# Kernel tuning notes

Hardware: AMD Instinct MI355X
Metric: run time of the kernel (lower is better)

The kernel has to match this reference:

```python
import jax, jax.numpy as jnp
import numpy as np

B = 16384
F_IN = 768
F_OUT = 512

def setup_inputs() -> dict:
    key = jax.random.key(0)
    k1, k2, k3, k4, k5, k6 = jax.random.split(key, 6)
    # densified sparse multi-hot boards (post to_dense())
    stm = jax.random.uniform(k1, (B, F_IN), dtype=jnp.float32)
    nstm = jax.random.uniform(k2, (B, F_IN), dtype=jnp.float32)
    s1 = 1.0 / np.sqrt(F_IN)
    s2 = 1.0 / np.sqrt(2 * F_OUT)
    W1 = jax.random.normal(k3, (F_OUT, F_IN), dtype=jnp.float32) * s1
    b1 = jax.random.normal(k4, (F_OUT,), dtype=jnp.float32) * s1
    W2 = jax.random.normal(k5, (1, 2 * F_OUT), dtype=jnp.float32) * s2
    b2 = jax.random.normal(k6, (1,), dtype=jnp.float32) * s2
    return {"stm": stm, "nstm": nstm, "W1": W1, "b1": b1, "W2": W2, "b2": b2}

def reference(stm, nstm, W1, b1, W2, b2):
    # shared feature transformer applied to both perspectives
    stm_p = stm @ W1.T + b1    # [B, F_OUT]
    nstm_p = nstm @ W1.T + b1  # [B, F_OUT]
    hidden = jnp.clip(jnp.concatenate((stm_p, nstm_p), axis=1), 0.0, 1.0)  # [B, 2*F_OUT]
    return jax.nn.sigmoid(hidden @ W2.T + b2)  # [B, 1]
```

## Files before the change

kernel.cpp:

```cpp
#include <hip/hip_runtime.h>
#include <hip/hip_bf16.h>

#define BATCH 16384
#define FIN   768
#define FOUT  512

#define BK 64
#define NT (FIN / BK)
#define BM 128
#define BN 256

typedef __attribute__((ext_vector_type(8))) short short8;
typedef __attribute__((ext_vector_type(4))) float floatx4;

__device__ __forceinline__ unsigned int cvt_pk_bf16(float a, float b) {
    unsigned int r;
    asm("v_cvt_pk_bf16_f32 %0, %1, %2" : "=v"(r) : "v"(a), "v"(b));
    return r;
}

__device__ __forceinline__ void load_lds_16(const void* g, void* l) {
    __builtin_amdgcn_global_load_lds(
        (const __attribute__((address_space(1))) unsigned int*)g,
        (__attribute__((address_space(3))) unsigned int*)l,
        16, 0, 0);
}

__global__ __launch_bounds__(256) void cvt_w1(
    const float* __restrict__ W1, unsigned short* __restrict__ W1b)
{
    int base = (blockIdx.x * 256 + threadIdx.x) * 8;
    float4 a = *(const float4*)(W1 + base);
    float4 b = *(const float4*)(W1 + base + 4);
    uint4 o;
    o.x = cvt_pk_bf16(a.x, a.y); o.y = cvt_pk_bf16(a.z, a.w);
    o.z = cvt_pk_bf16(b.x, b.y); o.w = cvt_pk_bf16(b.z, b.w);
    *(uint4*)(W1b + base) = o;
}

__global__ __launch_bounds__(1024, 4) void pn_gemm(
    const float* __restrict__ stm, const float* __restrict__ nstm,
    const unsigned short* __restrict__ W1b, const float* __restrict__ b1,
    const float* __restrict__ W2, float* __restrict__ P)
{
    __shared__ __align__(16) unsigned short As[2][256 * 64];
    __shared__ __align__(16) unsigned short Bs[2][256 * 64];

    const int tid  = threadIdx.x;
    const int lane = tid & 63;
    const int wave = tid >> 6;
    const int wr   = wave >> 2;
    const int wc   = wave & 3;
    const int quad = lane >> 4;
    const int l16  = lane & 15;

    const int bm    = blockIdx.x >> 1;
    const int n_idx = blockIdx.x & 1;
    const int b0    = bm * BM;
    const int n0    = n_idx * BN;

    const int arow = tid >> 2;
    const int ac   = tid & 3;
    const float* aSrc =
        ((arow < BM) ? stm  + (size_t)(b0 + arow) * FIN
                     : nstm + (size_t)(b0 + arow - BM) * FIN);
    const int aOffLo = arow * 64 + ((ac       ^ (arow & 7)) * 8);
    const int aOffHi = arow * 64 + (((ac + 4) ^ (arow & 7)) * 8);

    const int brow = lane >> 3;
    const int bch  = (lane & 7) ^ brow;
    const unsigned short* bSrc =
        W1b + (size_t)(n0 + brow) * FIN + bch * 8;

    floatx4 acc[4][4];
    #pragma unroll
    for (int i = 0; i < 4; ++i)
        #pragma unroll
        for (int j = 0; j < 4; ++j)
            acc[i][j] = (floatx4)0.0f;

    float4 ap0 = *(const float4*)(aSrc + ac * 8);
    float4 ap1 = *(const float4*)(aSrc + ac * 8 + 4);
    float4 ap2 = *(const float4*)(aSrc + (ac + 4) * 8);
    float4 ap3 = *(const float4*)(aSrc + (ac + 4) * 8 + 4);
    #pragma unroll
    for (int i = 0; i < 2; ++i) {
        const int J = wave * 2 + i;
        load_lds_16(bSrc + (size_t)(J * 8) * FIN, &Bs[0][J * 512]);
    }

    for (int t = 0; t < NT; ++t) {
        const int cur = t & 1;
        const int nxt = cur ^ 1;

        {
            uint4 o1, o2;
            o1.x = cvt_pk_bf16(ap0.x, ap0.y); o1.y = cvt_pk_bf16(ap0.z, ap0.w);
            o1.z = cvt_pk_bf16(ap1.x, ap1.y); o1.w = cvt_pk_bf16(ap1.z, ap1.w);
            o2.x = cvt_pk_bf16(ap2.x, ap2.y); o2.y = cvt_pk_bf16(ap2.z, ap2.w);
            o2.z = cvt_pk_bf16(ap3.x, ap3.y); o2.w = cvt_pk_bf16(ap3.z, ap3.w);
            *(uint4*)(&As[cur][aOffLo]) = o1;
            *(uint4*)(&As[cur][aOffHi]) = o2;
        }
        __syncthreads();

        if (t + 1 < NT) {
            const int kn = (t + 1) * BK;
            #pragma unroll
            for (int i = 0; i < 2; ++i) {
                const int J = wave * 2 + i;
                load_lds_16(bSrc + (size_t)(J * 8) * FIN + kn, &Bs[nxt][J * 512]);
            }
            ap0 = *(const float4*)(aSrc + kn + ac * 8);
            ap1 = *(const float4*)(aSrc + kn + ac * 8 + 4);
            ap2 = *(const float4*)(aSrc + kn + (ac + 4) * 8);
            ap3 = *(const float4*)(aSrc + kn + (ac + 4) * 8 + 4);
        }

        #pragma unroll
        for (int kk = 0; kk < 2; ++kk) {
            const int c = kk * 4 + quad;
            short8 af[4], bfr[4];
            #pragma unroll
            for (int mi = 0; mi < 4; ++mi) {
                const int m = wr * 64 + mi * 16 + l16;
                af[mi] = *(const short8*)(&As[cur][m * 64 + ((c ^ (m & 7)) * 8)]);
            }
            #pragma unroll
            for (int ni = 0; ni < 4; ++ni) {
                const int n = wc * 64 + ni * 16 + l16;
                bfr[ni] = *(const short8*)(&Bs[cur][n * 64 + ((c ^ (n & 7)) * 8)]);
            }
            #pragma unroll
            for (int mi = 0; mi < 4; ++mi)
                #pragma unroll
                for (int ni = 0; ni < 4; ++ni)
                    acc[mi][ni] = __builtin_amdgcn_mfma_f32_16x16x32_bf16(
                        af[mi], bfr[ni], acc[mi][ni], 0, 0, 0);
        }
    }

    float b1v[4], w2v[4];
    const float* w2base = (wr < 2) ? W2 : W2 + FOUT;
    #pragma unroll
    for (int ni = 0; ni < 4; ++ni) {
        int col = n0 + wc * 64 + ni * 16 + l16;
        b1v[ni] = b1[col];
        w2v[ni] = w2base[col];
    }

    __syncthreads();
    float* Epi = (float*)As;

    #pragma unroll
    for (int mi = 0; mi < 4; ++mi) {
        #pragma unroll
        for (int r = 0; r < 4; ++r) {
            float s = 0.0f;
            #pragma unroll
            for (int ni = 0; ni < 4; ++ni) {
                float h = acc[mi][ni][r] + b1v[ni];
                h = fminf(fmaxf(h, 0.0f), 1.0f);
                s += h * w2v[ni];
            }
            s += __shfl_xor(s, 1);
            s += __shfl_xor(s, 2);
            s += __shfl_xor(s, 4);
            s += __shfl_xor(s, 8);
            if (l16 == 0) {
                Epi[(wr * 64 + mi * 16 + quad * 4 + r) * 4 + wc] = s;
            }
        }
    }
    __syncthreads();

    if (tid < BM) {
        float x = 0.0f;
        #pragma unroll
        for (int j = 0; j < 4; ++j)
            x += Epi[tid * 4 + j] + Epi[(tid + BM) * 4 + j];
        P[n_idx * BATCH + b0 + tid] = x;
    }
}

__global__ __launch_bounds__(256) void finish(
    const float* __restrict__ P, const float* __restrict__ b2,
    float* __restrict__ out)
{
    int i = blockIdx.x * 256 + threadIdx.x;
    float x = b2[0] + P[i] + P[BATCH + i];
    out[i] = 1.0f / (1.0f + expf(-x));
}

extern "C" void kernel_launch(void* const* d_in, const int* in_sizes, int n_in,
                              void* d_out, int out_size, void* d_ws, size_t ws_size,
                              hipStream_t stream)
{
    (void)in_sizes; (void)n_in; (void)out_size; (void)ws_size;
    const float* stm  = (const float*)d_in[0];
    const float* nstm = (const float*)d_in[1];
    const float* W1   = (const float*)d_in[2];
    const float* b1   = (const float*)d_in[3];
    const float* W2   = (const float*)d_in[4];
    const float* b2   = (const float*)d_in[5];
    float* out = (float*)d_out;
    unsigned short* W1b = (unsigned short*)d_ws;
    float* P = (float*)((char*)d_ws + FOUT * FIN * 2);

    cvt_w1<<<dim3((FOUT * FIN) / (256 * 8)), dim3(256), 0, stream>>>(W1, W1b);
    pn_gemm<<<dim3((BATCH / BM) * 2), dim3(1024), 0, stream>>>(
        stm, nstm, W1b, b1, W2, P);
    finish<<<dim3(BATCH / 256), dim3(256), 0, stream>>>(P, b2, out);
}
```

Measured before the change: 146.2 us.

## Halve block to 512 threads with 8x4 MFMA tiles per wave, remap block ids, set MFMA priority

Drops the GEMM block from 16 to 8 waves. Each wave now computes a 128x64 output tile (8x4 MFMA accumulators) and each thread loads twice as much of A and B per stage. This gives more reuse of the B fragments per LDS read and fewer waves competing per block. Block ids are remapped (blockIdx & 7)*32 + (blockIdx >> 3), likely to place related tiles on the same XCD for cache locality, and s_setprio is raised around the MFMA bursts. The cost is higher register pressure from 128 accumulator floats per thread, which could lower occupancy.

```diff
diff --git a/kernel.cpp b/kernel.cpp
--- a/kernel.cpp
+++ b/kernel.cpp
@@ -38,7 +38,7 @@
     *(uint4*)(W1b + base) = o;
 }
 
-__global__ __launch_bounds__(1024, 4) void pn_gemm(
+__global__ __launch_bounds__(512, 2) void pn_gemm(
     const float* __restrict__ stm, const float* __restrict__ nstm,
     const unsigned short* __restrict__ W1b, const float* __restrict__ b1,
     const float* __restrict__ W2, float* __restrict__ P)
@@ -54,38 +54,43 @@
     const int quad = lane >> 4;
     const int l16  = lane & 15;
 
-    const int bm    = blockIdx.x >> 1;
-    const int n_idx = blockIdx.x & 1;
+    const int sbid  = (blockIdx.x & 7) * 32 + (blockIdx.x >> 3);
+    const int bm    = sbid >> 1;
+    const int n_idx = sbid & 1;
     const int b0    = bm * BM;
     const int n0    = n_idx * BN;
 
-    const int arow = tid >> 2;
-    const int ac   = tid & 3;
+    const int arow = tid >> 1;
+    const int h    = tid & 1;
     const float* aSrc =
         ((arow < BM) ? stm  + (size_t)(b0 + arow) * FIN
-                     : nstm + (size_t)(b0 + arow - BM) * FIN);
-    const int aOffLo = arow * 64 + ((ac       ^ (arow & 7)) * 8);
-    const int aOffHi = arow * 64 + (((ac + 4) ^ (arow & 7)) * 8);
+                     : nstm + (size_t)(b0 + arow - BM) * FIN) + h * 32;
+    int aOff[4];
+    #pragma unroll
+    for (int c = 0; c < 4; ++c)
+        aOff[c] = arow * 64 + (((h * 4 + c) ^ (arow & 7)) * 8);
 
     const int brow = lane >> 3;
     const int bch  = (lane & 7) ^ brow;
     const unsigned short* bSrc =
         W1b + (size_t)(n0 + brow) * FIN + bch * 8;
 
-    floatx4 acc[4][4];
-    #pragma unroll
-    for (int i = 0; i < 4; ++i)
+    floatx4 acc[8][4];
+    #pragma unroll
+    for (int i = 0; i < 8; ++i)
         #pragma unroll
         for (int j = 0; j < 4; ++j)
             acc[i][j] = (floatx4)0.0f;
 
-    float4 ap0 = *(const float4*)(aSrc + ac * 8);
-    float4 ap1 = *(const float4*)(aSrc + ac * 8 + 4);
-    float4 ap2 = *(const float4*)(aSrc + (ac + 4) * 8);
-    float4 ap3 = *(const float4*)(aSrc + (ac + 4) * 8 + 4);
-    #pragma unroll
-    for (int i = 0; i < 2; ++i) {
-        const int J = wave * 2 + i;
+    float4 ap[8];
+    #pragma unroll
+    for (int c = 0; c < 4; ++c) {
+        ap[2 * c]     = *(const float4*)(aSrc + c * 8);
+        ap[2 * c + 1] = *(const float4*)(aSrc + c * 8 + 4);
+    }
+    #pragma unroll
+    for (int i = 0; i < 4; ++i) {
+        const int J = wave * 4 + i;
         load_lds_16(bSrc + (size_t)(J * 8) * FIN, &Bs[0][J * 512]);
     }
 
@@ -93,37 +98,38 @@
         const int cur = t & 1;
         const int nxt = cur ^ 1;
 
-        {
-            uint4 o1, o2;
-            o1.x = cvt_pk_bf16(ap0.x, ap0.y); o1.y = cvt_pk_bf16(ap0.z, ap0.w);
-            o1.z = cvt_pk_bf16(ap1.x, ap1.y); o1.w = cvt_pk_bf16(ap1.z, ap1.w);
-            o2.x = cvt_pk_bf16(ap2.x, ap2.y); o2.y = cvt_pk_bf16(ap2.z, ap2.w);
-            o2.z = cvt_pk_bf16(ap3.x, ap3.y); o2.w = cvt_pk_bf16(ap3.z, ap3.w);
-            *(uint4*)(&As[cur][aOffLo]) = o1;
-            *(uint4*)(&As[cur][aOffHi]) = o2;
+        #pragma unroll
+        for (int c = 0; c < 4; ++c) {
+            uint4 o;
+            o.x = cvt_pk_bf16(ap[2 * c].x, ap[2 * c].y);
+            o.y = cvt_pk_bf16(ap[2 * c].z, ap[2 * c].w);
+            o.z = cvt_pk_bf16(ap[2 * c + 1].x, ap[2 * c + 1].y);
+            o.w = cvt_pk_bf16(ap[2 * c + 1].z, ap[2 * c + 1].w);
+            *(uint4*)(&As[cur][aOff[c]]) = o;
         }
         __syncthreads();
 
         if (t + 1 < NT) {
             const int kn = (t + 1) * BK;
             #pragma unroll
-            for (int i = 0; i < 2; ++i) {
-                const int J = wave * 2 + i;
+            for (int c = 0; c < 4; ++c) {
+                ap[2 * c]     = *(const float4*)(aSrc + kn + c * 8);
+                ap[2 * c + 1] = *(const float4*)(aSrc + kn + c * 8 + 4);
+            }
+            #pragma unroll
+            for (int i = 0; i < 4; ++i) {
+                const int J = wave * 4 + i;
                 load_lds_16(bSrc + (size_t)(J * 8) * FIN + kn, &Bs[nxt][J * 512]);
             }
-            ap0 = *(const float4*)(aSrc + kn + ac * 8);
-            ap1 = *(const float4*)(aSrc + kn + ac * 8 + 4);
-            ap2 = *(const float4*)(aSrc + kn + (ac + 4) * 8);
-            ap3 = *(const float4*)(aSrc + kn + (ac + 4) * 8 + 4);
         }
 
         #pragma unroll
         for (int kk = 0; kk < 2; ++kk) {
             const int c = kk * 4 + quad;
-            short8 af[4], bfr[4];
-            #pragma unroll
-            for (int mi = 0; mi < 4; ++mi) {
-                const int m = wr * 64 + mi * 16 + l16;
+            short8 af[8], bfr[4];
+            #pragma unroll
+            for (int mi = 0; mi < 8; ++mi) {
+                const int m = wr * 128 + mi * 16 + l16;
                 af[mi] = *(const short8*)(&As[cur][m * 64 + ((c ^ (m & 7)) * 8)]);
             }
             #pragma unroll
@@ -131,17 +137,19 @@
                 const int n = wc * 64 + ni * 16 + l16;
                 bfr[ni] = *(const short8*)(&Bs[cur][n * 64 + ((c ^ (n & 7)) * 8)]);
             }
-            #pragma unroll
-            for (int mi = 0; mi < 4; ++mi)
+            __builtin_amdgcn_s_setprio(1);
+            #pragma unroll
+            for (int mi = 0; mi < 8; ++mi)
                 #pragma unroll
                 for (int ni = 0; ni < 4; ++ni)
                     acc[mi][ni] = __builtin_amdgcn_mfma_f32_16x16x32_bf16(
                         af[mi], bfr[ni], acc[mi][ni], 0, 0, 0);
+            __builtin_amdgcn_s_setprio(0);
         }
     }
 
     float b1v[4], w2v[4];
-    const float* w2base = (wr < 2) ? W2 : W2 + FOUT;
+    const float* w2base = (wr == 0) ? W2 : W2 + FOUT;
     #pragma unroll
     for (int ni = 0; ni < 4; ++ni) {
         int col = n0 + wc * 64 + ni * 16 + l16;
@@ -153,22 +161,22 @@
     float* Epi = (float*)As;
 
     #pragma unroll
-    for (int mi = 0; mi < 4; ++mi) {
+    for (int mi = 0; mi < 8; ++mi) {
         #pragma unroll
         for (int r = 0; r < 4; ++r) {
             float s = 0.0f;
             #pragma unroll
             for (int ni = 0; ni < 4; ++ni) {
-                float h = acc[mi][ni][r] + b1v[ni];
-                h = fminf(fmaxf(h, 0.0f), 1.0f);
-                s += h * w2v[ni];
+                float hh = acc[mi][ni][r] + b1v[ni];
+                hh = fminf(fmaxf(hh, 0.0f), 1.0f);
+                s += hh * w2v[ni];
             }
             s += __shfl_xor(s, 1);
             s += __shfl_xor(s, 2);
             s += __shfl_xor(s, 4);
             s += __shfl_xor(s, 8);
             if (l16 == 0) {
-                Epi[(wr * 64 + mi * 16 + quad * 4 + r) * 4 + wc] = s;
+                Epi[(wr * 128 + mi * 16 + quad * 4 + r) * 4 + wc] = s;
             }
         }
     }
@@ -208,7 +216,7 @@
     float* P = (float*)((char*)d_ws + FOUT * FIN * 2);
 
     cvt_w1<<<dim3((FOUT * FIN) / (256 * 8)), dim3(256), 0, stream>>>(W1, W1b);
-    pn_gemm<<<dim3((BATCH / BM) * 2), dim3(1024), 0, stream>>>(
+    pn_gemm<<<dim3((BATCH / BM) * 2), dim3(512), 0, stream>>>(
         stm, nstm, W1b, b1, W2, P);
     finish<<<dim3(BATCH / 256), dim3(256), 0, stream>>>(P, b2, out);
 }
```

New measurement: 163.7 us. 1.12x slower.

## Triple-buffer W1 tiles with prefetch distance two and swizzle block order

Applied to the files above, without the earlier changes.

Moves the W1 tile to three LDS buffers and issues its async global-to-LDS loads two k-steps ahead. The block barrier is replaced by a custom one that waits with vmcnt(2), so the newest B prefetch can stay in flight across the barrier. Block indices are also remapped so that neighbouring tiles spread across XCD groups. The aim is to hide global load latency of the B operand, at the cost of raising LDS use to 160KB and relying on a hand-counted vmcnt being correct.

```diff
diff --git a/kernel.cpp b/kernel.cpp
--- a/kernel.cpp
+++ b/kernel.cpp
@@ -25,6 +25,13 @@
         (__attribute__((address_space(3))) unsigned int*)l,
         16, 0, 0);
 }
+
+#define BAR_VM2() do {                                               \
+    __builtin_amdgcn_sched_barrier(0);                               \
+    asm volatile("s_waitcnt vmcnt(2) lgkmcnt(0)" ::: "memory");      \
+    __builtin_amdgcn_s_barrier();                                    \
+    __builtin_amdgcn_sched_barrier(0);                               \
+} while (0)
 
 __global__ __launch_bounds__(256) void cvt_w1(
     const float* __restrict__ W1, unsigned short* __restrict__ W1b)
@@ -44,7 +51,7 @@
     const float* __restrict__ W2, float* __restrict__ P)
 {
     __shared__ __align__(16) unsigned short As[2][256 * 64];
-    __shared__ __align__(16) unsigned short Bs[2][256 * 64];
+    __shared__ __align__(16) unsigned short Bs[3][256 * 64];
 
     const int tid  = threadIdx.x;
     const int lane = tid & 63;
@@ -54,8 +61,9 @@
     const int quad = lane >> 4;
     const int l16  = lane & 15;
 
-    const int bm    = blockIdx.x >> 1;
-    const int n_idx = blockIdx.x & 1;
+    const int sbid  = (blockIdx.x & 7) * 32 + (blockIdx.x >> 3);
+    const int bm    = sbid >> 1;
+    const int n_idx = sbid & 1;
     const int b0    = bm * BM;
     const int n0    = n_idx * BN;
 
@@ -79,6 +87,11 @@
         for (int j = 0; j < 4; ++j)
             acc[i][j] = (floatx4)0.0f;
 
+    #pragma unroll
+    for (int i = 0; i < 2; ++i) {
+        const int J = wave * 2 + i;
+        load_lds_16(bSrc + (size_t)(J * 8) * FIN, &Bs[0][J * 512]);
+    }
     float4 ap0 = *(const float4*)(aSrc + ac * 8);
     float4 ap1 = *(const float4*)(aSrc + ac * 8 + 4);
     float4 ap2 = *(const float4*)(aSrc + (ac + 4) * 8);
@@ -86,12 +99,12 @@
     #pragma unroll
     for (int i = 0; i < 2; ++i) {
         const int J = wave * 2 + i;
-        load_lds_16(bSrc + (size_t)(J * 8) * FIN, &Bs[0][J * 512]);
-    }
-
+        load_lds_16(bSrc + (size_t)(J * 8) * FIN + BK, &Bs[1][J * 512]);
+    }
+
+    int bc = 0;
     for (int t = 0; t < NT; ++t) {
         const int cur = t & 1;
-        const int nxt = cur ^ 1;
 
         {
             uint4 o1, o2;
@@ -102,20 +115,25 @@
             *(uint4*)(&As[cur][aOffLo]) = o1;
             *(uint4*)(&As[cur][aOffHi]) = o2;
         }
-        __syncthreads();
+        BAR_VM2();
 
         if (t + 1 < NT) {
             const int kn = (t + 1) * BK;
-            #pragma unroll
-            for (int i = 0; i < 2; ++i) {
-                const int J = wave * 2 + i;
-                load_lds_16(bSrc + (size_t)(J * 8) * FIN + kn, &Bs[nxt][J * 512]);
-            }
             ap0 = *(const float4*)(aSrc + kn + ac * 8);
             ap1 = *(const float4*)(aSrc + kn + ac * 8 + 4);
             ap2 = *(const float4*)(aSrc + kn + (ac + 4) * 8);
             ap3 = *(const float4*)(aSrc + kn + (ac + 4) * 8 + 4);
         }
+        if (t + 2 < NT) {
+            int bp = bc + 2; if (bp >= 3) bp -= 3;
+            const size_t kn2 = (size_t)(t + 2) * BK;
+            #pragma unroll
+            for (int i = 0; i < 2; ++i) {
+                const int J = wave * 2 + i;
+                load_lds_16(bSrc + (size_t)(J * 8) * FIN + kn2,
+                            &Bs[bp][J * 512]);
+            }
+        }
 
         #pragma unroll
         for (int kk = 0; kk < 2; ++kk) {
@@ -129,7 +147,7 @@
             #pragma unroll
             for (int ni = 0; ni < 4; ++ni) {
                 const int n = wc * 64 + ni * 16 + l16;
-                bfr[ni] = *(const short8*)(&Bs[cur][n * 64 + ((c ^ (n & 7)) * 8)]);
+                bfr[ni] = *(const short8*)(&Bs[bc][n * 64 + ((c ^ (n & 7)) * 8)]);
             }
             #pragma unroll
             for (int mi = 0; mi < 4; ++mi)
@@ -138,6 +156,8 @@
                     acc[mi][ni] = __builtin_amdgcn_mfma_f32_16x16x32_bf16(
                         af[mi], bfr[ni], acc[mi][ni], 0, 0, 0);
         }
+
+        bc = (bc == 2) ? 0 : bc + 1;
     }
 
     float b1v[4], w2v[4];
```

Measured after the change: 145.5 us. No clear change (-0.4%).

## Shrink GEMM tiles to 64x128 with 256-thread blocks and XCD-aware block swizzle

Applied to the files above, without the earlier changes.

Block tile drops from 128 rows per perspective x 256 columns x 64 K to 64 x 128 x 32, and blocks go from 1024 to 256 threads. This raises the block count, cuts LDS use per block, and reorders block IDs so neighbouring tiles land on the same XCD. The aim is more occupancy and better L2 locality. In exchange, each byte loaded is reused less, and with four column partitions every input row is reread four times from global memory, plus the finish kernel now sums four partials.

```diff
diff --git a/kernel.cpp b/kernel.cpp
--- a/kernel.cpp
+++ b/kernel.cpp
@@ -5,10 +5,10 @@
 #define FIN   768
 #define FOUT  512
 
-#define BK 64
+#define BK 32
 #define NT (FIN / BK)
-#define BM 128
-#define BN 256
+#define BMB 64
+#define BN 128
 
 typedef __attribute__((ext_vector_type(8))) short short8;
 typedef __attribute__((ext_vector_type(4))) float floatx4;
@@ -38,37 +38,38 @@
     *(uint4*)(W1b + base) = o;
 }
 
-__global__ __launch_bounds__(1024, 4) void pn_gemm(
+__global__ __launch_bounds__(256, 4) void pn_gemm(
     const float* __restrict__ stm, const float* __restrict__ nstm,
     const unsigned short* __restrict__ W1b, const float* __restrict__ b1,
     const float* __restrict__ W2, float* __restrict__ P)
 {
-    __shared__ __align__(16) unsigned short As[2][256 * 64];
-    __shared__ __align__(16) unsigned short Bs[2][256 * 64];
+    __shared__ __align__(16) unsigned short As[2][128 * 32];
+    __shared__ __align__(16) unsigned short Bs[2][128 * 32];
 
     const int tid  = threadIdx.x;
     const int lane = tid & 63;
     const int wave = tid >> 6;
-    const int wr   = wave >> 2;
-    const int wc   = wave & 3;
+    const int wr   = wave >> 1;
+    const int wc   = wave & 1;
     const int quad = lane >> 4;
     const int l16  = lane & 15;
 
-    const int bm    = blockIdx.x >> 1;
-    const int n_idx = blockIdx.x & 1;
-    const int b0    = bm * BM;
+    const int sbid  = (blockIdx.x & 7) * 128 + (blockIdx.x >> 3);
+    const int bm    = sbid >> 2;
+    const int n_idx = sbid & 3;
+    const int b0    = bm * BMB;
     const int n0    = n_idx * BN;
 
-    const int arow = tid >> 2;
-    const int ac   = tid & 3;
+    const int arow = tid >> 1;
+    const int ac   = tid & 1;
     const float* aSrc =
-        ((arow < BM) ? stm  + (size_t)(b0 + arow) * FIN
-                     : nstm + (size_t)(b0 + arow - BM) * FIN);
-    const int aOffLo = arow * 64 + ((ac       ^ (arow & 7)) * 8);
-    const int aOffHi = arow * 64 + (((ac + 4) ^ (arow & 7)) * 8);
-
-    const int brow = lane >> 3;
-    const int bch  = (lane & 7) ^ brow;
+        ((arow < BMB) ? stm  + (size_t)(b0 + arow) * FIN
+                      : nstm + (size_t)(b0 + arow - BMB) * FIN);
+    const int aOffLo = arow * 32 + ((ac       ^ (arow & 3)) * 8);
+    const int aOffHi = arow * 32 + (((ac + 2) ^ (arow & 3)) * 8);
+
+    const int brow = lane >> 2;
+    const int bch  = (lane & 3) ^ (brow & 3);
     const unsigned short* bSrc =
         W1b + (size_t)(n0 + brow) * FIN + bch * 8;
 
@@ -81,12 +82,12 @@
 
     float4 ap0 = *(const float4*)(aSrc + ac * 8);
     float4 ap1 = *(const float4*)(aSrc + ac * 8 + 4);
-    float4 ap2 = *(const float4*)(aSrc + (ac + 4) * 8);
-    float4 ap3 = *(const float4*)(aSrc + (ac + 4) * 8 + 4);
+    float4 ap2 = *(const float4*)(aSrc + (ac + 2) * 8);
+    float4 ap3 = *(const float4*)(aSrc + (ac + 2) * 8 + 4);
     #pragma unroll
     for (int i = 0; i < 2; ++i) {
         const int J = wave * 2 + i;
-        load_lds_16(bSrc + (size_t)(J * 8) * FIN, &Bs[0][J * 512]);
+        load_lds_16(bSrc + (size_t)(J * 16) * FIN, &Bs[0][J * 512]);
     }
 
     for (int t = 0; t < NT; ++t) {
@@ -109,27 +110,27 @@
             #pragma unroll
             for (int i = 0; i < 2; ++i) {
                 const int J = wave * 2 + i;
-                load_lds_16(bSrc + (size_t)(J * 8) * FIN + kn, &Bs[nxt][J * 512]);
+                load_lds_16(bSrc + (size_t)(J * 16) * FIN + kn,
+                            &Bs[nxt][J * 512]);
             }
             ap0 = *(const float4*)(aSrc + kn + ac * 8);
             ap1 = *(const float4*)(aSrc + kn + ac * 8 + 4);
-            ap2 = *(const float4*)(aSrc + kn + (ac + 4) * 8);
-            ap3 = *(const float4*)(aSrc + kn + (ac + 4) * 8 + 4);
-        }
-
-        #pragma unroll
-        for (int kk = 0; kk < 2; ++kk) {
-            const int c = kk * 4 + quad;
+            ap2 = *(const float4*)(aSrc + kn + (ac + 2) * 8);
+            ap3 = *(const float4*)(aSrc + kn + (ac + 2) * 8 + 4);
+        }
+
+        {
+            const int c = quad;
             short8 af[4], bfr[4];
             #pragma unroll
             for (int mi = 0; mi < 4; ++mi) {
                 const int m = wr * 64 + mi * 16 + l16;
-                af[mi] = *(const short8*)(&As[cur][m * 64 + ((c ^ (m & 7)) * 8)]);
+                af[mi] = *(const short8*)(&As[cur][m * 32 + ((c ^ (m & 3)) * 8)]);
             }
             #pragma unroll
             for (int ni = 0; ni < 4; ++ni) {
                 const int n = wc * 64 + ni * 16 + l16;
-                bfr[ni] = *(const short8*)(&Bs[cur][n * 64 + ((c ^ (n & 7)) * 8)]);
+                bfr[ni] = *(const short8*)(&Bs[cur][n * 32 + ((c ^ (n & 3)) * 8)]);
             }
             #pragma unroll
             for (int mi = 0; mi < 4; ++mi)
@@ -141,7 +142,7 @@
     }
 
     float b1v[4], w2v[4];
-    const float* w2base = (wr < 2) ? W2 : W2 + FOUT;
+    const float* w2base = (wr == 0) ? W2 : W2 + FOUT;
     #pragma unroll
     for (int ni = 0; ni < 4; ++ni) {
         int col = n0 + wc * 64 + ni * 16 + l16;
@@ -168,17 +169,15 @@
             s += __shfl_xor(s, 4);
             s += __shfl_xor(s, 8);
             if (l16 == 0) {
-                Epi[(wr * 64 + mi * 16 + quad * 4 + r) * 4 + wc] = s;
+                Epi[(wr * 64 + mi * 16 + quad * 4 + r) * 2 + wc] = s;
             }
         }
     }
     __syncthreads();
 
-    if (tid < BM) {
-        float x = 0.0f;
-        #pragma unroll
-        for (int j = 0; j < 4; ++j)
-            x += Epi[tid * 4 + j] + Epi[(tid + BM) * 4 + j];
+    if (tid < BMB) {
+        float x = Epi[tid * 2] + Epi[tid * 2 + 1]
+                + Epi[(tid + BMB) * 2] + Epi[(tid + BMB) * 2 + 1];
         P[n_idx * BATCH + b0 + tid] = x;
     }
 }
@@ -188,7 +187,7 @@
     float* __restrict__ out)
 {
     int i = blockIdx.x * 256 + threadIdx.x;
-    float x = b2[0] + P[i] + P[BATCH + i];
+    float x = b2[0] + P[i] + P[BATCH + i] + P[2 * BATCH + i] + P[3 * BATCH + i];
     out[i] = 1.0f / (1.0f + expf(-x));
 }
 
@@ -208,7 +207,7 @@
     float* P = (float*)((char*)d_ws + FOUT * FIN * 2);
 
     cvt_w1<<<dim3((FOUT * FIN) / (256 * 8)), dim3(256), 0, stream>>>(W1, W1b);
-    pn_gemm<<<dim3((BATCH / BM) * 2), dim3(1024), 0, stream>>>(
+    pn_gemm<<<dim3((BATCH / BMB) * 4), dim3(256), 0, stream>>>(
         stm, nstm, W1b, b1, W2, P);
     finish<<<dim3(BATCH / 256), dim3(256), 0, stream>>>(P, b2, out);
 }
```

After: 168.1 us. 1.15x slower.
